# Kernel optimization log

Measured on AMD Instinct MI355X. Metric: run time of the kernel, lower is better.

## Reference

```python
import jax, jax.numpy as jnp
import numpy as np

N = 100000
E = 1600000
IN_F = 128
HIDDEN = 128
HEADS = 2
N_CLASSES = 40
NEG_SLOPE = 0.2
BN_EPS = 1e-5


def setup_inputs() -> dict:
    key = jax.random.key(0)
    ks = jax.random.split(key, 12)
    c1 = HIDDEN // HEADS  # 64
    c2 = N_CLASSES        # 40 per head, concat=False
    inp = {
        "x": jax.random.normal(ks[0], (N, IN_F), dtype=jnp.float32),
        "edge_index": jax.random.randint(ks[1], (2, E), 0, N, dtype=jnp.int32),
        # layer 1 GATConv params
        "W1": jax.random.normal(ks[2], (IN_F, HEADS * c1), dtype=jnp.float32) * 0.05,
        "att_src1": jax.random.normal(ks[3], (HEADS, c1), dtype=jnp.float32) * 0.05,
        "att_dst1": jax.random.normal(ks[4], (HEADS, c1), dtype=jnp.float32) * 0.05,
        "b1": jnp.zeros((HEADS * c1,), dtype=jnp.float32),
        # BatchNorm params
        "gamma": jnp.ones((HIDDEN,), dtype=jnp.float32),
        "beta": jnp.zeros((HIDDEN,), dtype=jnp.float32),
        # layer 2 GATConv params (concat=False)
        "W2": jax.random.normal(ks[5], (HIDDEN, HEADS * c2), dtype=jnp.float32) * 0.05,
        "att_src2": jax.random.normal(ks[6], (HEADS, c2), dtype=jnp.float32) * 0.05,
        "att_dst2": jax.random.normal(ks[7], (HEADS, c2), dtype=jnp.float32) * 0.05,
        "b2": jnp.zeros((c2,), dtype=jnp.float32),
    }
    return inp


def gat_conv(x, src, dst, W, att_src, att_dst, bias, heads, concat):
    n = x.shape[0]
    h = (x @ W).reshape(n, heads, -1)             # [N, H, C]
    a_src = jnp.sum(h * att_src[None], axis=-1)   # [N, H]
    a_dst = jnp.sum(h * att_dst[None], axis=-1)   # [N, H]
    alpha = jax.nn.leaky_relu(a_src[src] + a_dst[dst], NEG_SLOPE)  # [E, H]
    # numerically-stable segment softmax over edges grouped by dst
    amax = jax.ops.segment_max(alpha, dst, num_segments=n)
    e = jnp.exp(alpha - amax[dst])
    denom = jax.ops.segment_sum(e, dst, num_segments=n)
    w = e / denom[dst]                            # [E, H]
    msg = h[src] * w[:, :, None]                  # [E, H, C]
    out = jax.ops.segment_sum(msg, dst, num_segments=n)  # [N, H, C]
    if concat:
        out = out.reshape(n, -1)
    else:
        out = out.mean(axis=1)
    return out + bias


def batch_norm(x, gamma, beta):
    mean = x.mean(axis=0)
    var = x.var(axis=0)
    return (x - mean) * jax.lax.rsqrt(var + BN_EPS) * gamma + beta


def reference(x, edge_index, W1, att_src1, att_dst1, b1, gamma, beta,
              W2, att_src2, att_dst2, b2):
    n = x.shape[0]
    # PyG GATConv default: add self-loops
    loops = jnp.arange(n, dtype=edge_index.dtype)
    src = jnp.concatenate([edge_index[0], loops])
    dst = jnp.concatenate([edge_index[1], loops])
    h = gat_conv(x, src, dst, W1, att_src1, att_dst1, b1, HEADS, concat=True)
    h = batch_norm(h, gamma, beta)
    h = gat_conv(h, src, dst, W2, att_src2, att_dst2, b2, HEADS, concat=False)
    return jax.nn.log_softmax(h, axis=1)
```

## Files before the change

### kernel.cpp

```cpp
#include <hip/hip_runtime.h>
#include <hip/hip_bf16.h>
#include <hip/hip_fp16.h>
#include <stdint.h>

#define N_NODES 100000
#define N_EDGES 1600000
#define ET (N_EDGES + N_NODES)
#define HID 128
#define C2 40
#define F2 80
#define NEG 0.2f
#define BN_EPS 1e-5f
#define NBUCK 391
#define BCAP 6144
#define NBB 640
#define EPB ((ET + NBB - 1) / NBB)
#define CHK 512

typedef __hip_bfloat16 bf16;
typedef __attribute__((ext_vector_type(8))) short s8v;
typedef __attribute__((ext_vector_type(4))) float f4v;
typedef __attribute__((ext_vector_type(4))) unsigned int u4v;
typedef __attribute__((ext_vector_type(2))) unsigned int u2v;

__device__ __forceinline__ float b2f(bf16 v){ return __bfloat162float(v); }
__device__ __forceinline__ float rdf(const void* p, size_t i, int isb){
    return isb ? b2f(((const bf16*)p)[i]) : ((const float*)p)[i];
}
__device__ __forceinline__ unsigned short f2bb(float v){
    bf16 h = __float2bfloat16(v);
    return *(unsigned short*)&h;
}
__device__ __forceinline__ uint32_t pack2(float a, float b){
    return (uint32_t)f2bb(a) | ((uint32_t)f2bb(b) << 16);
}
__device__ __forceinline__ uint32_t packh2(float a, float b){
    return (uint32_t)__half_as_ushort(__float2half(a))
         | ((uint32_t)__half_as_ushort(__float2half(b)) << 16);
}
__device__ __forceinline__ float lo16(uint32_t u){ return __uint_as_float(u << 16); }
__device__ __forceinline__ float hi16(uint32_t u){ return __uint_as_float(u & 0xFFFF0000u); }
__device__ __forceinline__ float hcvt(uint32_t w, int sh){
    return __half2float(__ushort_as_half((unsigned short)((w >> sh) & 0xFFFFu)));
}

__global__ __launch_bounds__(256) void k_init(
    const uint32_t* __restrict__ w1bits, int* __restrict__ flag,
    int* __restrict__ gcur, float* __restrict__ stats)
{
    __shared__ int cnt;
    int t = threadIdx.x;
    if (t == 0) cnt = 0;
    __syncthreads();
    uint32_t b = w1bits[t];
    float lo = __uint_as_float((b & 0xFFFFu) << 16);
    float a = fabsf(lo);
    if (a > 1e-8f && a < 1.0f) atomicAdd(&cnt, 1);
    for (int i = t; i < NBUCK; i += 256) gcur[i] = 0;
    stats[t] = 0.f;
    __syncthreads();
    if (t == 0) *flag = (cnt >= 192) ? 1 : 0;
}

__global__ __launch_bounds__(256) void k_gemm1(
    const void* __restrict__ x, const void* __restrict__ W1,
    const void* __restrict__ attS, const void* __restrict__ attD,
    const int* __restrict__ flag, unsigned short* __restrict__ h1,
    float* __restrict__ aS, float* __restrict__ aD)
{
    __shared__ __attribute__((aligned(16))) unsigned short wT[128*132];
    const int isb = *flag;
    const int tid = threadIdx.x;
    if (isb) {
        const unsigned short* w = (const unsigned short*)W1;
        for (int idx = tid; idx < 128*128; idx += 256){
            int k = idx >> 7, n = idx & 127;
            wT[n*132 + k] = w[idx];
        }
    } else {
        const float* w = (const float*)W1;
        for (int idx = tid; idx < 128*128; idx += 256){
            int k = idx >> 7, n = idx & 127;
            wT[n*132 + k] = f2bb(w[idx]);
        }
    }
    __syncthreads();

    const int w4 = tid >> 6, lane = tid & 63, quad = lane >> 4, l16 = lane & 15;
    const int rowbase = blockIdx.x*32 + (w4 >> 1)*16;
    const int colbase = (w4 & 1)*64;
    const int head = w4 & 1;

    s8v bfr[4][4];
    float asv[4], adv[4];
    #pragma unroll
    for (int ct = 0; ct < 4; ct++){
        int n = colbase + ct*16 + l16;
        asv[ct] = rdf(attS, n, isb);
        adv[ct] = rdf(attD, n, isb);
        #pragma unroll
        for (int s = 0; s < 4; s++){
            int k0 = s*32 + quad*8;
            const unsigned short* p = &wT[n*132 + k0];
            u2v a = *(const u2v*)p, b = *(const u2v*)(p+4);
            union { u4v u; s8v s; } cv; cv.u = (u4v){a[0],a[1],b[0],b[1]};
            bfr[ct][s] = cv.s;
        }
    }

    f4v acc[4];
    #pragma unroll
    for (int ct = 0; ct < 4; ct++) acc[ct] = (f4v){0.f,0.f,0.f,0.f};

    const int m = rowbase + l16;
    #pragma unroll
    for (int s = 0; s < 4; s++){
        int k0 = s*32 + quad*8;
        s8v af;
        if (isb){
            union { u4v u; s8v s; } cv;
            cv.u = *(const u4v*)((const unsigned short*)x + (size_t)m*128 + k0);
            af = cv.s;
        } else {
            const float* xp = (const float*)x + (size_t)m*128 + k0;
            f4v f0 = *(const f4v*)xp, f1 = *(const f4v*)(xp+4);
            union { u4v u; s8v s; } cv;
            cv.u = (u4v){pack2(f0[0],f0[1]), pack2(f0[2],f0[3]),
                         pack2(f1[0],f1[1]), pack2(f1[2],f1[3])};
            af = cv.s;
        }
        #pragma unroll
        for (int ct = 0; ct < 4; ct++)
            acc[ct] = __builtin_amdgcn_mfma_f32_16x16x32_bf16(af, bfr[ct][s], acc[ct], 0,0,0);
    }

    #pragma unroll
    for (int ct = 0; ct < 4; ct++){
        int col = colbase + ct*16 + l16;
        #pragma unroll
        for (int r = 0; r < 4; r++){
            int row = rowbase + quad*4 + r;
            h1[(size_t)row*128 + col] = f2bb(acc[ct][r]);
        }
    }

    #pragma unroll
    for (int r = 0; r < 4; r++){
        float vs = 0.f, vd = 0.f;
        #pragma unroll
        for (int ct = 0; ct < 4; ct++){ vs += acc[ct][r]*asv[ct]; vd += acc[ct][r]*adv[ct]; }
        #pragma unroll
        for (int o = 1; o < 16; o <<= 1){
            vs += __shfl_xor(vs, o, 64);
            vd += __shfl_xor(vd, o, 64);
        }
        if (l16 == 0){
            int row = rowbase + quad*4 + r;
            aS[row*2 + head] = vs;
            aD[row*2 + head] = vd;
        }
    }
}

__global__ __launch_bounds__(256) void k_bin(
    const int* __restrict__ esrc, const int* __restrict__ edst,
    int* __restrict__ gcur, uint32_t* __restrict__ staging)
{
    __shared__ int cnt[NBUCK];
    __shared__ int bb[NBUCK];
    const int t = threadIdx.x;
    for (int i = t; i < NBUCK; i += 256) cnt[i] = 0;
    __syncthreads();
    const int e0 = blockIdx.x * EPB;
    const int e1 = (e0 + EPB < ET) ? e0 + EPB : ET;
    for (int e = e0 + t; e < e1; e += 256){
        int d = (e < N_EDGES) ? edst[e] : e - N_EDGES;
        atomicAdd(&cnt[d >> 8], 1);
    }
    __syncthreads();
    const int bofs = (int)(blockIdx.x % NBUCK);
    for (int i = t; i < NBUCK; i += 256){
        int bkt = i + bofs; if (bkt >= NBUCK) bkt -= NBUCK;
        int c = cnt[bkt];
        bb[bkt] = c ? atomicAdd(&gcur[bkt], c) : 0;
        cnt[bkt] = 0;
    }
    __syncthreads();
    for (int e = e0 + t; e < e1; e += 256){
        int d, s;
        if (e < N_EDGES){ s = esrc[e]; d = edst[e]; } else { s = d = e - N_EDGES; }
        int b = d >> 8;
        int r = atomicAdd(&cnt[b], 1);
        int p = bb[b] + r;
        if (p < BCAP) staging[(size_t)b*BCAP + p] = ((uint32_t)s << 8) | (uint32_t)(d & 255);
    }
}

__global__ __launch_bounds__(256) void k_sort(
    const int* __restrict__ gcur, const uint32_t* __restrict__ staging,
    int* __restrict__ deg, int* __restrict__ cur, int* __restrict__ eidx)
{
    __shared__ int h[256], sc[256], rk[256];
    __shared__ int lsrc[BCAP];
    const int b = blockIdx.x;
    const int t = threadIdx.x;
    const int base = b * BCAP;
    int cnt = gcur[b];
    if (cnt > BCAP) cnt = BCAP;
    h[t] = 0; rk[t] = 0;
    __syncthreads();
    for (int i = t; i < cnt; i += 256)
        atomicAdd(&h[staging[base + i] & 255u], 1);
    __syncthreads();
    sc[t] = h[t];
    __syncthreads();
    for (int off = 1; off < 256; off <<= 1){
        int v = (t >= off) ? sc[t - off] : 0;
        __syncthreads();
        sc[t] += v;
        __syncthreads();
    }
    int dg = b*256 + t;
    if (dg < N_NODES){
        deg[dg] = h[t];
        cur[dg] = base + sc[t];
    }
    __syncthreads();
    for (int i = t; i < cnt; i += 256){
        uint32_t w = staging[base + i];
        int dl = w & 255u;
        int r = atomicAdd(&rk[dl], 1);
        lsrc[sc[dl] - h[dl] + r] = (int)(w >> 8);
    }
    __syncthreads();
    for (int i = t; i < cnt; i += 256) eidx[base + i] = lsrc[i];
}

__global__ __launch_bounds__(256) void k_agg1(
    const int* __restrict__ cur, const int* __restrict__ deg,
    const int* __restrict__ eidx, const float* __restrict__ aS,
    const float* __restrict__ aD, const uint32_t* __restrict__ h1u,
    uint32_t* __restrict__ out1u)
{
    __shared__ uint2 lse[4][CHK + 8];
    const int wv = threadIdx.x >> 6;
    int d = blockIdx.x*4 + wv;
    if (d >= N_NODES) return;
    const int l = threadIdx.x & 63;
    const int c = l & 15;
    const int g = l >> 4;
    const uint32_t c16 = (uint32_t)(c*16);
    int end   = __builtin_amdgcn_readfirstlane(cur[d]);
    int start = end - __builtin_amdgcn_readfirstlane(deg[d]);
    float2 ad = *(const float2*)(aD + d*2);
    const int sh = (c >= 8) ? 16 : 0;
    float den0 = 0.f, den1 = 0.f;
    float acc[8];
    #pragma unroll
    for (int k = 0; k < 8; k++) acc[k] = 0.f;
    const char* hb = (const char*)h1u;

#define G1(P, W) { u4v Gx = *(const u4v*)(hb + ((P).x + c16)); \
    float Wf = (W); \
    acc[0] += Wf*lo16(Gx[0]); acc[1] += Wf*hi16(Gx[0]); \
    acc[2] += Wf*lo16(Gx[1]); acc[3] += Wf*hi16(Gx[1]); \
    acc[4] += Wf*lo16(Gx[2]); acc[5] += Wf*hi16(Gx[2]); \
    acc[6] += Wf*lo16(Gx[3]); acc[7] += Wf*hi16(Gx[3]); }

    for (int c0 = start; c0 < end; c0 += CHK){
        int c1 = (c0 + CHK < end) ? c0 + CHK : end;
        int n = c1 - c0;
        for (int j = c0 + l; j < c1; j += 64){
            int s = eidx[j];
            float2 as = *(const float2*)((const char*)aS + ((uint32_t)s*8u));
            float al0 = as.x + ad.x, al1 = as.y + ad.y;
            al0 = al0 > 0.f ? al0 : NEG*al0;
            al1 = al1 > 0.f ? al1 : NEG*al1;
            float e0 = __expf(al0), e1 = __expf(al1);
            lse[wv][j - c0] = make_uint2((uint32_t)s << 8, packh2(e0, e1));
            den0 += e0; den1 += e1;
        }
        int nn = (n + 3) & ~3;
        if (l < nn - n) lse[wv][n + l] = make_uint2(0u, 0u);
        int i = 0;
        for (; i + 16 <= nn; i += 16){
            uint2 pa = lse[wv][i + g];
            uint2 pb = lse[wv][i + 4 + g];
            uint2 pc = lse[wv][i + 8 + g];
            uint2 pd = lse[wv][i + 12 + g];
            G1(pa, hcvt(pa.y, sh));
            G1(pb, hcvt(pb.y, sh));
            G1(pc, hcvt(pc.y, sh));
            G1(pd, hcvt(pd.y, sh));
        }
        for (; i < nn; i += 4){
            uint2 pa = lse[wv][i + g];
            G1(pa, hcvt(pa.y, sh));
        }
    }
#undef G1
    #pragma unroll
    for (int o = 1; o < 64; o <<= 1){
        den0 += __shfl_xor(den0, o, 64);
        den1 += __shfl_xor(den1, o, 64);
    }
    #pragma unroll
    for (int k = 0; k < 8; k++){
        acc[k] += __shfl_xor(acc[k], 32, 64);
        acc[k] += __shfl_xor(acc[k], 16, 64);
    }
    float r = 1.f / fmaxf((c < 8) ? den0 : den1, 1e-20f);
    if (l < 16){
        u4v o;
        #pragma unroll
        for (int q = 0; q < 4; q++) o[q] = pack2(acc[2*q]*r, acc[2*q+1]*r);
        *(u4v*)(out1u + (size_t)d*64 + 4*c) = o;
    }
}

__global__ __launch_bounds__(256) void k_bnstats(
    const uint32_t* __restrict__ out1u, float* __restrict__ stats)
{
    __shared__ float red[4][64][4];
    int fp = threadIdx.x & 63;
    int wv = threadIdx.x >> 6;
    float s0 = 0.f, q0 = 0.f, s1 = 0.f, q1 = 0.f;
    for (int r = blockIdx.x*4 + wv; r < N_NODES; r += 512){
        uint32_t u = out1u[(size_t)r*64 + fp];
        float f0 = lo16(u), f1 = hi16(u);
        s0 += f0; q0 += f0*f0; s1 += f1; q1 += f1*f1;
    }
    red[wv][fp][0] = s0; red[wv][fp][1] = s1;
    red[wv][fp][2] = q0; red[wv][fp][3] = q1;
    __syncthreads();
    if (threadIdx.x < 64){
        int l = threadIdx.x;
        float a0=0.f, a1=0.f, b0=0.f, b1=0.f;
        #pragma unroll
        for (int w = 0; w < 4; w++){
            a0 += red[w][l][0]; a1 += red[w][l][1];
            b0 += red[w][l][2]; b1 += red[w][l][3];
        }
        unsafeAtomicAdd(&stats[2*l],       a0);
        unsafeAtomicAdd(&stats[2*l+1],     a1);
        unsafeAtomicAdd(&stats[128+2*l],   b0);
        unsafeAtomicAdd(&stats[128+2*l+1], b1);
    }
}

__global__ __launch_bounds__(256) void k_gemm2(
    const unsigned short* __restrict__ out1b, const float* __restrict__ stats,
    const void* __restrict__ gamma, const void* __restrict__ beta,
    const void* __restrict__ W2, const void* __restrict__ attS,
    const void* __restrict__ attD, const int* __restrict__ flag,
    unsigned short* __restrict__ h2, float* __restrict__ aS, float* __restrict__ aD)
{
    __shared__ __attribute__((aligned(16))) unsigned short wT[80*132];
    __shared__ float scl[128], shl[128];
    const int isb = *flag;
    const int tid = threadIdx.x;
    for (int idx = tid; idx < 128*80; idx += 256){
        int k = idx / 80, n = idx - k*80;
        wT[n*132 + k] = isb ? ((const unsigned short*)W2)[idx]
                            : f2bb(((const float*)W2)[idx]);
    }
    if (tid < 128){
        float mean = stats[tid] * (1.f / N_NODES);
        float var = fmaxf(stats[128+tid] * (1.f / N_NODES) - mean*mean, 0.f);
        float rs = rsqrtf(var + BN_EPS);
        float sc = rdf(gamma, tid, isb) * rs;
        scl[tid] = sc;
        shl[tid] = rdf(beta, tid, isb) - mean*sc;
    }
    __syncthreads();

    const int w4 = tid >> 6, lane = tid & 63, quad = lane >> 4, l16 = lane & 15;
    const int rowbase = blockIdx.x*64 + w4*16;

    s8v bfr[5][4];
    float asv[5], adv[5];
    #pragma unroll
    for (int ct = 0; ct < 5; ct++){
        int n = ct*16 + l16;
        asv[ct] = rdf(attS, n, isb);
        adv[ct] = rdf(attD, n, isb);
        #pragma unroll
        for (int s = 0; s < 4; s++){
            int k0 = s*32 + quad*8;
            const unsigned short* p = &wT[n*132 + k0];
            u2v a = *(const u2v*)p, b = *(const u2v*)(p+4);
            union { u4v u; s8v s; } cv; cv.u = (u4v){a[0],a[1],b[0],b[1]};
            bfr[ct][s] = cv.s;
        }
    }

    f4v acc[5];
    #pragma unroll
    for (int ct = 0; ct < 5; ct++) acc[ct] = (f4v){0.f,0.f,0.f,0.f};

    int m = rowbase + l16;
    int mc = m < N_NODES ? m : N_NODES - 1;
    #pragma unroll
    for (int s = 0; s < 4; s++){
        int k0 = s*32 + quad*8;
        union { u4v u; s8v s8; } cin;
        cin.u = *(const u4v*)(out1b + (size_t)mc*128 + k0);
        u4v up;
        #pragma unroll
        for (int i = 0; i < 4; i++){
            float f0 = lo16(cin.u[i]), f1 = hi16(cin.u[i]);
            int k = k0 + 2*i;
            up[i] = pack2(f0*scl[k] + shl[k], f1*scl[k+1] + shl[k+1]);
        }
        union { u4v u; s8v s8; } cv; cv.u = up;
        #pragma unroll
        for (int ct = 0; ct < 5; ct++)
            acc[ct] = __builtin_amdgcn_mfma_f32_16x16x32_bf16(cv.s8, bfr[ct][s], acc[ct], 0,0,0);
    }

    #pragma unroll
    for (int ct = 0; ct < 5; ct++){
        int col = ct*16 + l16;
        #pragma unroll
        for (int r = 0; r < 4; r++){
            int row = rowbase + quad*4 + r;
            if (row < N_NODES) h2[(size_t)row*80 + col] = f2bb(acc[ct][r]);
        }
    }

    #pragma unroll
    for (int r = 0; r < 4; r++){
        float vs0 = 0.f, vs1 = 0.f, vd0 = 0.f, vd1 = 0.f;
        #pragma unroll
        for (int ct = 0; ct < 5; ct++){
            int col = ct*16 + l16;
            float ps = acc[ct][r]*asv[ct], pd = acc[ct][r]*adv[ct];
            if (col < 40){ vs0 += ps; vd0 += pd; } else { vs1 += ps; vd1 += pd; }
        }
        #pragma unroll
        for (int o = 1; o < 16; o <<= 1){
            vs0 += __shfl_xor(vs0, o, 64); vs1 += __shfl_xor(vs1, o, 64);
            vd0 += __shfl_xor(vd0, o, 64); vd1 += __shfl_xor(vd1, o, 64);
        }
        if (l16 == 0){
            int row = rowbase + quad*4 + r;
            if (row < N_NODES){
                aS[row*2 + 0] = vs0; aS[row*2 + 1] = vs1;
                aD[row*2 + 0] = vd0; aD[row*2 + 1] = vd1;
            }
        }
    }
}

__global__ __launch_bounds__(256) void k_agg2(
    const int* __restrict__ cur, const int* __restrict__ deg,
    const int* __restrict__ eidx, const float* __restrict__ aS,
    const float* __restrict__ aD, const uint32_t* __restrict__ h2u,
    const void* __restrict__ b2v, const int* __restrict__ flag,
    void* __restrict__ out)
{
    __shared__ uint2 lse[4][CHK + 8];
    const int wv = threadIdx.x >> 6;
    int d = blockIdx.x*4 + wv;
    if (d >= N_NODES) return;
    const int l = threadIdx.x & 63;
    const int isb = *flag;
    const int c = l % 10;
    const int g = l / 10;
    const bool act = l < 60;
    const int gq = act ? g : 0;
    const uint32_t c16 = (uint32_t)(c*16);
    int end   = __builtin_amdgcn_readfirstlane(cur[d]);
    int start = end - __builtin_amdgcn_readfirstlane(deg[d]);
    float2 ad = *(const float2*)(aD + d*2);
    const int sh = (c >= 5) ? 16 : 0;
    float den0 = 0.f, den1 = 0.f;
    float acc[8];
    #pragma unroll
    for (int k = 0; k < 8; k++) acc[k] = 0.f;
    const char* hb = (const char*)h2u;

#define G2(P, W) { u4v Gx = *(const u4v*)(hb + ((P).x + c16)); \
    float Wf = (W); \
    acc[0] += Wf*lo16(Gx[0]); acc[1] += Wf*hi16(Gx[0]); \
    acc[2] += Wf*lo16(Gx[1]); acc[3] += Wf*hi16(Gx[1]); \
    acc[4] += Wf*lo16(Gx[2]); acc[5] += Wf*hi16(Gx[2]); \
    acc[6] += Wf*lo16(Gx[3]); acc[7] += Wf*hi16(Gx[3]); }

    for (int c0 = start; c0 < end; c0 += CHK){
        int c1 = (c0 + CHK < end) ? c0 + CHK : end;
        int n = c1 - c0;
        for (int j = c0 + l; j < c1; j += 64){
            int s = eidx[j];
            float2 as = *(const float2*)((const char*)aS + ((uint32_t)s*8u));
            float al0 = as.x + ad.x, al1 = as.y + ad.y;
            al0 = al0 > 0.f ? al0 : NEG*al0;
            al1 = al1 > 0.f ? al1 : NEG*al1;
            float e0 = __expf(al0), e1 = __expf(al1);
            lse[wv][j - c0] = make_uint2((uint32_t)s * 160u, packh2(e0, e1));
            den0 += e0; den1 += e1;
        }
        int nn = ((n + 5) / 6) * 6;
        if (l < nn - n) lse[wv][n + l] = make_uint2(0u, 0u);
        int i = 0;
        for (; i + 18 <= nn; i += 18){
            uint2 pa = lse[wv][i + gq];
            uint2 pb = lse[wv][i + 6 + gq];
            uint2 pc = lse[wv][i + 12 + gq];
            G2(pa, act ? hcvt(pa.y, sh) : 0.f);
            G2(pb, act ? hcvt(pb.y, sh) : 0.f);
            G2(pc, act ? hcvt(pc.y, sh) : 0.f);
        }
        for (; i < nn; i += 6){
            uint2 pa = lse[wv][i + gq];
            G2(pa, act ? hcvt(pa.y, sh) : 0.f);
        }
    }
#undef G2
    #pragma unroll
    for (int o = 1; o < 64; o <<= 1){
        den0 += __shfl_xor(den0, o, 64);
        den1 += __shfl_xor(den1, o, 64);
    }
    #pragma unroll
    for (int k = 0; k < 8; k++)
        acc[k] += __shfl(acc[k], l + 30, 64);
    #pragma unroll
    for (int k = 0; k < 8; k++)
        acc[k] += __shfl(acc[k], l + 20, 64) + __shfl(acc[k], l + 10, 64);
    float r = 1.f / fmaxf((c < 5) ? den0 : den1, 1e-20f);
    #pragma unroll
    for (int k = 0; k < 8; k++) acc[k] *= r;

    int lb = (l < 5) ? l : 0;
    float v[8];
    float mx = -1e30f;
    #pragma unroll
    for (int k = 0; k < 8; k++){
        float t = __shfl(acc[k], l + 5, 64);
        v[k] = 0.5f*(acc[k] + t) + rdf(b2v, 8*lb + k, isb);
        mx = fmaxf(mx, v[k]);
    }
    if (l >= 5) mx = -1e30f;
    mx = fmaxf(mx, __shfl_xor(mx, 1, 64));
    mx = fmaxf(mx, __shfl_xor(mx, 2, 64));
    mx = fmaxf(mx, __shfl_xor(mx, 4, 64));
    float ex = 0.f;
    if (l < 5){
        #pragma unroll
        for (int k = 0; k < 8; k++) ex += __expf(v[k] - mx);
    }
    ex += __shfl_xor(ex, 1, 64);
    ex += __shfl_xor(ex, 2, 64);
    ex += __shfl_xor(ex, 4, 64);
    float lsf = __logf(ex);
    if (l < 5){
        if (isb){
            u4v o;
            #pragma unroll
            for (int q = 0; q < 4; q++)
                o[q] = pack2(v[2*q] - mx - lsf, v[2*q+1] - mx - lsf);
            *(u4v*)((uint32_t*)out + (size_t)d*20 + 4*l) = o;
        } else {
            float4 o0, o1;
            o0.x = v[0]-mx-lsf; o0.y = v[1]-mx-lsf; o0.z = v[2]-mx-lsf; o0.w = v[3]-mx-lsf;
            o1.x = v[4]-mx-lsf; o1.y = v[5]-mx-lsf; o1.z = v[6]-mx-lsf; o1.w = v[7]-mx-lsf;
            ((float4*)out)[(size_t)d*10 + 2*l]     = o0;
            ((float4*)out)[(size_t)d*10 + 2*l + 1] = o1;
        }
    }
}

extern "C" void kernel_launch(void* const* d_in, const int* in_sizes, int n_in,
                              void* d_out, int out_size, void* d_ws, size_t ws_size,
                              hipStream_t stream)
{
    const void* x    = d_in[0];
    const int*  ei   = (const int*)d_in[1];
    const void* W1   = d_in[2];
    const void* as1  = d_in[3];
    const void* ad1  = d_in[4];
    const void* gamma = d_in[6];
    const void* beta  = d_in[7];
    const void* W2   = d_in[8];
    const void* as2  = d_in[9];
    const void* ad2  = d_in[10];
    const void* b2v  = d_in[11];
    const int* esrc = ei;
    const int* edst = ei + N_EDGES;

    char* ws = (char*)d_ws;
    size_t off = 0;
    auto alloc = [&](size_t bytes) {
        void* p = ws + off;
        off += (bytes + 255) & ~(size_t)255;
        return p;
    };
    int*   flag  = (int*)alloc(256);
    float* stats = (float*)alloc(sizeof(float)*256);
    int*   gcur  = (int*)alloc(sizeof(int)*NBUCK);
    float* aS1   = (float*)alloc(sizeof(float)*N_NODES*2);
    float* aD1   = (float*)alloc(sizeof(float)*N_NODES*2);
    float* aS2   = (float*)alloc(sizeof(float)*N_NODES*2);
    float* aD2   = (float*)alloc(sizeof(float)*N_NODES*2);
    int*   deg   = (int*)alloc(sizeof(int)*N_NODES);
    int*   cur   = (int*)alloc(sizeof(int)*N_NODES);
    uint32_t* staging = (uint32_t*)alloc(sizeof(uint32_t)*(size_t)NBUCK*BCAP);
    int*   eidx  = (int*)alloc(sizeof(int)*(size_t)NBUCK*BCAP);
    unsigned short* h1  = (unsigned short*)alloc(2*(size_t)N_NODES*HID);
    unsigned short* out1 = (unsigned short*)alloc(2*(size_t)N_NODES*HID);
    unsigned short* h2  = h1;

    k_init<<<1, 256, 0, stream>>>((const uint32_t*)W1, flag, gcur, stats);
    k_gemm1<<<3125, 256, 0, stream>>>(x, W1, as1, ad1, flag, h1, aS1, aD1);
    k_bin<<<NBB, 256, 0, stream>>>(esrc, edst, gcur, staging);
    k_sort<<<NBUCK, 256, 0, stream>>>(gcur, staging, deg, cur, eidx);
    k_agg1<<<25000, 256, 0, stream>>>(cur, deg, eidx, aS1, aD1,
                                      (const uint32_t*)h1, (uint32_t*)out1);
    k_bnstats<<<128, 256, 0, stream>>>((const uint32_t*)out1, stats);
    k_gemm2<<<1563, 256, 0, stream>>>(out1, stats, gamma, beta, W2, as2, ad2,
                                      flag, h2, aS2, aD2);
    k_agg2<<<25000, 256, 0, stream>>>(cur, deg, eidx, aS2, aD2,
                                      (const uint32_t*)h2, b2v, flag, d_out);
}
```

Baseline: 427.8 us.

## Process two destination nodes per wavefront in GAT aggregation kernels

Both aggregation kernels now split each 64-lane wavefront into two 32-lane halves, each handling its own destination node, which halves the grid. Average degree is about 17, so a full wavefront per node left many lanes idle in the edge-scoring phase and needed extra cross-lane reductions. The cost is divergence when the two nodes in a wave have different degrees, since the wave runs until the longer one finishes. Loop bounds are now per-lane values rather than wave-uniform readfirstlane results, and the shared-memory chunk is halved per node.

Measured after the change: 412.7 us. -3.5%, faster.

```diff
diff --git a/kernel.cpp b/kernel.cpp
--- a/kernel.cpp
+++ b/kernel.cpp
@@ -15,7 +15,7 @@
 #define BCAP 6144
 #define NBB 640
 #define EPB ((ET + NBB - 1) / NBB)
-#define CHK 512
+#define CH2 256
 
 typedef __hip_bfloat16 bf16;
 typedef __attribute__((ext_vector_type(8))) short s8v;
@@ -242,16 +242,16 @@
     const float* __restrict__ aD, const uint32_t* __restrict__ h1u,
     uint32_t* __restrict__ out1u)
 {
-    __shared__ uint2 lse[4][CHK + 8];
+    __shared__ uint2 lse[4][2][CH2 + 4];
     const int wv = threadIdx.x >> 6;
-    int d = blockIdx.x*4 + wv;
-    if (d >= N_NODES) return;
     const int l = threadIdx.x & 63;
-    const int c = l & 15;
-    const int g = l >> 4;
+    const int half = l >> 5, ll = l & 31;
+    const int d = blockIdx.x*8 + wv*2 + half;
+    const int c = ll & 15;
+    const int g = ll >> 4;
     const uint32_t c16 = (uint32_t)(c*16);
-    int end   = __builtin_amdgcn_readfirstlane(cur[d]);
-    int start = end - __builtin_amdgcn_readfirstlane(deg[d]);
+    int end   = cur[d];
+    int start = end - deg[d];
     float2 ad = *(const float2*)(aD + d*2);
     const int sh = (c >= 8) ? 16 : 0;
     float den0 = 0.f, den1 = 0.f;
@@ -267,50 +267,48 @@
     acc[4] += Wf*lo16(Gx[2]); acc[5] += Wf*hi16(Gx[2]); \
     acc[6] += Wf*lo16(Gx[3]); acc[7] += Wf*hi16(Gx[3]); }
 
-    for (int c0 = start; c0 < end; c0 += CHK){
-        int c1 = (c0 + CHK < end) ? c0 + CHK : end;
+    for (int c0 = start; c0 < end; c0 += CH2){
+        int c1 = (c0 + CH2 < end) ? c0 + CH2 : end;
         int n = c1 - c0;
-        for (int j = c0 + l; j < c1; j += 64){
+        for (int j = c0 + ll; j < c1; j += 32){
             int s = eidx[j];
             float2 as = *(const float2*)((const char*)aS + ((uint32_t)s*8u));
             float al0 = as.x + ad.x, al1 = as.y + ad.y;
             al0 = al0 > 0.f ? al0 : NEG*al0;
             al1 = al1 > 0.f ? al1 : NEG*al1;
             float e0 = __expf(al0), e1 = __expf(al1);
-            lse[wv][j - c0] = make_uint2((uint32_t)s << 8, packh2(e0, e1));
+            lse[wv][half][j - c0] = make_uint2((uint32_t)s << 8, packh2(e0, e1));
             den0 += e0; den1 += e1;
         }
-        int nn = (n + 3) & ~3;
-        if (l < nn - n) lse[wv][n + l] = make_uint2(0u, 0u);
+        int nn = (n + 1) & ~1;
+        if (ll < nn - n) lse[wv][half][n + ll] = make_uint2(0u, 0u);
         int i = 0;
-        for (; i + 16 <= nn; i += 16){
-            uint2 pa = lse[wv][i + g];
-            uint2 pb = lse[wv][i + 4 + g];
-            uint2 pc = lse[wv][i + 8 + g];
-            uint2 pd = lse[wv][i + 12 + g];
+        for (; i + 8 <= nn; i += 8){
+            uint2 pa = lse[wv][half][i + g];
+            uint2 pb = lse[wv][half][i + 2 + g];
+            uint2 pc = lse[wv][half][i + 4 + g];
+            uint2 pd = lse[wv][half][i + 6 + g];
             G1(pa, hcvt(pa.y, sh));
             G1(pb, hcvt(pb.y, sh));
             G1(pc, hcvt(pc.y, sh));
             G1(pd, hcvt(pd.y, sh));
         }
-        for (; i < nn; i += 4){
-            uint2 pa = lse[wv][i + g];
+        for (; i < nn; i += 2){
+            uint2 pa = lse[wv][half][i + g];
             G1(pa, hcvt(pa.y, sh));
         }
     }
 #undef G1
     #pragma unroll
-    for (int o = 1; o < 64; o <<= 1){
+    for (int o = 1; o < 32; o <<= 1){
         den0 += __shfl_xor(den0, o, 64);
         den1 += __shfl_xor(den1, o, 64);
     }
     #pragma unroll
-    for (int k = 0; k < 8; k++){
-        acc[k] += __shfl_xor(acc[k], 32, 64);
+    for (int k = 0; k < 8; k++)
         acc[k] += __shfl_xor(acc[k], 16, 64);
-    }
     float r = 1.f / fmaxf((c < 8) ? den0 : den1, 1e-20f);
-    if (l < 16){
+    if (ll < 16){
         u4v o;
         #pragma unroll
         for (int q = 0; q < 4; q++) o[q] = pack2(acc[2*q]*r, acc[2*q+1]*r);
@@ -459,19 +457,19 @@
     const void* __restrict__ b2v, const int* __restrict__ flag,
     void* __restrict__ out)
 {
-    __shared__ uint2 lse[4][CHK + 8];
+    __shared__ uint2 lse[4][2][CH2 + 4];
     const int wv = threadIdx.x >> 6;
-    int d = blockIdx.x*4 + wv;
-    if (d >= N_NODES) return;
     const int l = threadIdx.x & 63;
+    const int half = l >> 5, ll = l & 31;
+    const int d = blockIdx.x*8 + wv*2 + half;
     const int isb = *flag;
-    const int c = l % 10;
-    const int g = l / 10;
-    const bool act = l < 60;
+    const int c = ll % 10;
+    const int g = ll / 10;
+    const bool act = ll < 30;
     const int gq = act ? g : 0;
     const uint32_t c16 = (uint32_t)(c*16);
-    int end   = __builtin_amdgcn_readfirstlane(cur[d]);
-    int start = end - __builtin_amdgcn_readfirstlane(deg[d]);
+    int end   = cur[d];
+    int start = end - deg[d];
     float2 ad = *(const float2*)(aD + d*2);
     const int sh = (c >= 5) ? 16 : 0;
     float den0 = 0.f, den1 = 0.f;
@@ -487,52 +485,49 @@
     acc[4] += Wf*lo16(Gx[2]); acc[5] += Wf*hi16(Gx[2]); \
     acc[6] += Wf*lo16(Gx[3]); acc[7] += Wf*hi16(Gx[3]); }
 
-    for (int c0 = start; c0 < end; c0 += CHK){
-        int c1 = (c0 + CHK < end) ? c0 + CHK : end;
+    for (int c0 = start; c0 < end; c0 += CH2){
+        int c1 = (c0 + CH2 < end) ? c0 + CH2 : end;
         int n = c1 - c0;
-        for (int j = c0 + l; j < c1; j += 64){
+        for (int j = c0 + ll; j < c1; j += 32){
             int s = eidx[j];
             float2 as = *(const float2*)((const char*)aS + ((uint32_t)s*8u));
             float al0 = as.x + ad.x, al1 = as.y + ad.y;
             al0 = al0 > 0.f ? al0 : NEG*al0;
             al1 = al1 > 0.f ? al1 : NEG*al1;
             float e0 = __expf(al0), e1 = __expf(al1);
-            lse[wv][j - c0] = make_uint2((uint32_t)s * 160u, packh2(e0, e1));
+            lse[wv][half][j - c0] = make_uint2((uint32_t)s * 160u, packh2(e0, e1));
             den0 += e0; den1 += e1;
         }
-        int nn = ((n + 5) / 6) * 6;
-        if (l < nn - n) lse[wv][n + l] = make_uint2(0u, 0u);
+        int nn = ((n + 2) / 3) * 3;
+        if (ll < nn - n) lse[wv][half][n + ll] = make_uint2(0u, 0u);
         int i = 0;
-        for (; i + 18 <= nn; i += 18){
-            uint2 pa = lse[wv][i + gq];
-            uint2 pb = lse[wv][i + 6 + gq];
-            uint2 pc = lse[wv][i + 12 + gq];
+        for (; i + 9 <= nn; i += 9){
+            uint2 pa = lse[wv][half][i + gq];
+            uint2 pb = lse[wv][half][i + 3 + gq];
+            uint2 pc = lse[wv][half][i + 6 + gq];
             G2(pa, act ? hcvt(pa.y, sh) : 0.f);
             G2(pb, act ? hcvt(pb.y, sh) : 0.f);
             G2(pc, act ? hcvt(pc.y, sh) : 0.f);
         }
-        for (; i < nn; i += 6){
-            uint2 pa = lse[wv][i + gq];
+        for (; i < nn; i += 3){
+            uint2 pa = lse[wv][half][i + gq];
             G2(pa, act ? hcvt(pa.y, sh) : 0.f);
         }
     }
 #undef G2
     #pragma unroll
-    for (int o = 1; o < 64; o <<= 1){
+    for (int o = 1; o < 32; o <<= 1){
         den0 += __shfl_xor(den0, o, 64);
         den1 += __shfl_xor(den1, o, 64);
     }
     #pragma unroll
     for (int k = 0; k < 8; k++)
-        acc[k] += __shfl(acc[k], l + 30, 64);
-    #pragma unroll
-    for (int k = 0; k < 8; k++)
-        acc[k] += __shfl(acc[k], l + 20, 64) + __shfl(acc[k], l + 10, 64);
+        acc[k] += __shfl(acc[k], l + 10, 64) + __shfl(acc[k], l + 20, 64);
     float r = 1.f / fmaxf((c < 5) ? den0 : den1, 1e-20f);
     #pragma unroll
     for (int k = 0; k < 8; k++) acc[k] *= r;
 
-    int lb = (l < 5) ? l : 0;
+    int lb = (ll < 5) ? ll : 0;
     float v[8];
     float mx = -1e30f;
     #pragma unroll
@@ -541,12 +536,12 @@
         v[k] = 0.5f*(acc[k] + t) + rdf(b2v, 8*lb + k, isb);
         mx = fmaxf(mx, v[k]);
     }
-    if (l >= 5) mx = -1e30f;
+    if (ll >= 5) mx = -1e30f;
     mx = fmaxf(mx, __shfl_xor(mx, 1, 64));
     mx = fmaxf(mx, __shfl_xor(mx, 2, 64));
     mx = fmaxf(mx, __shfl_xor(mx, 4, 64));
     float ex = 0.f;
-    if (l < 5){
+    if (ll < 5){
         #pragma unroll
         for (int k = 0; k < 8; k++) ex += __expf(v[k] - mx);
     }
@@ -554,19 +549,19 @@
     ex += __shfl_xor(ex, 2, 64);
     ex += __shfl_xor(ex, 4, 64);
     float lsf = __logf(ex);
-    if (l < 5){
+    if (ll < 5){
         if (isb){
             u4v o;
             #pragma unroll
             for (int q = 0; q < 4; q++)
                 o[q] = pack2(v[2*q] - mx - lsf, v[2*q+1] - mx - lsf);
-            *(u4v*)((uint32_t*)out + (size_t)d*20 + 4*l) = o;
+            *(u4v*)((uint32_t*)out + (size_t)d*20 + 4*ll) = o;
         } else {
             float4 o0, o1;
             o0.x = v[0]-mx-lsf; o0.y = v[1]-mx-lsf; o0.z = v[2]-mx-lsf; o0.w = v[3]-mx-lsf;
             o1.x = v[4]-mx-lsf; o1.y = v[5]-mx-lsf; o1.z = v[6]-mx-lsf; o1.w = v[7]-mx-lsf;
-            ((float4*)out)[(size_t)d*10 + 2*l]     = o0;
-            ((float4*)out)[(size_t)d*10 + 2*l + 1] = o1;
+            ((float4*)out)[(size_t)d*10 + 2*ll]     = o0;
+            ((float4*)out)[(size_t)d*10 + 2*ll + 1] = o1;
         }
     }
 }
@@ -615,11 +610,11 @@
     k_gemm1<<<3125, 256, 0, stream>>>(x, W1, as1, ad1, flag, h1, aS1, aD1);
     k_bin<<<NBB, 256, 0, stream>>>(esrc, edst, gcur, staging);
     k_sort<<<NBUCK, 256, 0, stream>>>(gcur, staging, deg, cur, eidx);
-    k_agg1<<<25000, 256, 0, stream>>>(cur, deg, eidx, aS1, aD1,
+    k_agg1<<<12500, 256, 0, stream>>>(cur, deg, eidx, aS1, aD1,
                                       (const uint32_t*)h1, (uint32_t*)out1);
     k_bnstats<<<128, 256, 0, stream>>>((const uint32_t*)out1, stats);
     k_gemm2<<<1563, 256, 0, stream>>>(out1, stats, gamma, beta, W2, as2, ad2,
                                       flag, h2, aS2, aD2);
-    k_agg2<<<25000, 256, 0, stream>>>(cur, deg, eidx, aS2, aD2,
+    k_agg2<<<12500, 256, 0, stream>>>(cur, deg, eidx, aS2, aD2,
                                       (const uint32_t*)h2, b2v, flag, d_out);
 }
```
